# Optimization experiments

Measured on AMD Instinct MI355X. Metric: run time of the kernel, lower is better.

Reference implementation:

```python
import jax, jax.numpy as jnp
import numpy as np

DIM = 128      # encoder output dim
D_OUT = 10     # num classes
T = 1.0        # temperature
EPS = 1e-7


def setup_inputs() -> dict:
    key = jax.random.key(0)
    ks = jax.random.split(key, 5)
    B, N, D_IN = 512, 100000, 128
    x = jax.random.normal(ks[0], (B, D_IN), jnp.float32)
    candidate_x = jax.random.normal(ks[1], (N, D_IN), jnp.float32)
    candidate_y = jax.random.randint(ks[2], (N,), 0, D_OUT, dtype=jnp.int32)
    W = jax.random.normal(ks[3], (DIM, D_IN), jnp.float32) / np.sqrt(D_IN).astype(np.float32)
    b = jax.random.normal(ks[4], (DIM,), jnp.float32) * 0.01
    return {"x": x, "candidate_x": candidate_x, "candidate_y": candidate_y, "W": W, "b": b}


def reference(x, candidate_x, candidate_y, W, b):
    # Linear encoder (n_blocks == 0 path)
    h = x @ W.T + b              # [B, DIM]
    hc = candidate_x @ W.T + b   # [N, DIM]
    # Pairwise L2 distances via the Gram expansion (same math as torch.cdist p=2)
    d2 = (jnp.sum(h * h, axis=-1, keepdims=True)
          + jnp.sum(hc * hc, axis=-1)[None, :]
          - 2.0 * (h @ hc.T))    # [B, N]
    dist = jnp.sqrt(jnp.maximum(d2, 0.0)) / T
    # Attention-like masked softmax over candidates (eval: no diagonal mask)
    p = jax.nn.softmax(-dist, axis=-1)              # [B, N]
    onehot_y = jax.nn.one_hot(candidate_y, D_OUT, dtype=p.dtype)  # [N, D_OUT]
    logits = p @ onehot_y                           # [B, D_OUT]
    return jnp.log(logits + EPS)
```

## Files before the change

### kernel.cpp

```cpp
#include <hip/hip_runtime.h>
#include <stdint.h>

typedef __bf16 bf16x8 __attribute__((ext_vector_type(8)));
typedef float f32x4 __attribute__((ext_vector_type(4)));
typedef short short8 __attribute__((ext_vector_type(8)));
typedef unsigned int uint2v __attribute__((ext_vector_type(2)));
typedef float float4_t __attribute__((ext_vector_type(4)));

#define LOG2E 1.44269504088896340736f

union FragU { short8 s; bf16x8 b; };
union YbU { uint2v u2[2]; bf16x8 b; };

#define DEVI static __device__ __forceinline__

DEVI f32x4 mfma16(bf16x8 a, bf16x8 b, f32x4 c) {
  return __builtin_amdgcn_mfma_f32_16x16x32_bf16(a, b, c, 0, 0, 0);
}

DEVI bf16x8 cvt8(float4_t a, float4_t b) {
  bf16x8 r;
  r[0] = (__bf16)a[0]; r[1] = (__bf16)a[1]; r[2] = (__bf16)a[2]; r[3] = (__bf16)a[3];
  r[4] = (__bf16)b[0]; r[5] = (__bf16)b[1]; r[6] = (__bf16)b[2]; r[7] = (__bf16)b[3];
  return r;
}

__global__ __launch_bounds__(256, 3) void prep_encode_kernel(
    const float* __restrict__ cx, const float* __restrict__ x,
    const float* __restrict__ W, const float* __restrict__ bias,
    const int* __restrict__ y,
    unsigned short* __restrict__ HC, float* __restrict__ hcn,
    unsigned short* __restrict__ Hm, float* __restrict__ hnm,
    unsigned short* __restrict__ YT,
    int N, int Bm, int NP, int NBA, int NBB, int bpc) {
  __shared__ __align__(16) unsigned short Wl[128 * 128];

  const int bid = blockIdx.x, t = threadIdx.x;
  const int NB_ENC = NBA + NBB;

  if (bid >= NB_ENC) {
    if (bid == NB_ENC) {
      int i = N + t;
      if (i < NP) hcn[i] = 1e30f;
    } else {
      int k = bid - NB_ENC - 1;
      int c = k / bpc, j = k - c * bpc;
      int n0 = j * 2048 + t * 8;
      unsigned short* dst = YT + (size_t)c * NP + n0;
#pragma unroll
      for (int e = 0; e < 8; ++e) {
        int n = n0 + e;
        if (n < NP) dst[e] = (n < N && y[n] == c) ? 0x3F80u : 0u;
      }
    }
    return;
  }

  const float* in;
  unsigned short* outh;
  float* outnorm;
  int M, blk;
  if (bid < NBA) {
    in = cx; outh = HC; outnorm = hcn; M = N; blk = bid;
  } else {
    in = x; outh = Hm; outnorm = hnm; M = Bm; blk = bid - NBA;
  }

  const int lane = t & 63, w = t >> 6;
  const int g = lane >> 4, q = lane & 15;
  const int rb = blk * 128 + w * 16;

  float4_t iv[2][8];
  int arow[2];
  bool av[2];
#pragma unroll
  for (int s = 0; s < 2; ++s) {
    arow[s] = rb + s * 64 + q;
    av[s] = arow[s] < M;
    int ar = av[s] ? arow[s] : 0;
    const float* src = in + (size_t)ar * 128 + g * 8;
#pragma unroll
    for (int kc = 0; kc < 4; ++kc) {
      iv[s][2 * kc] = *(const float4_t*)(src + kc * 32);
      iv[s][2 * kc + 1] = *(const float4_t*)(src + kc * 32 + 4);
    }
  }

  {
    int row = t >> 1, half = t & 1;
    const float* wsrc = W + row * 128 + half * 64;
    float4_t wv[16];
#pragma unroll
    for (int j = 0; j < 16; ++j) wv[j] = *(const float4_t*)(wsrc + j * 4);
#pragma unroll
    for (int j = 0; j < 8; ++j) {
      FragU u; u.b = cvt8(wv[2 * j], wv[2 * j + 1]);
      int slot = (half * 8 + j) ^ (row & 7);
      *(short8*)((char*)Wl + row * 256 + slot * 16) = u.s;
    }
  }
  __syncthreads();

  bf16x8 a[2][4];
#pragma unroll
  for (int s = 0; s < 2; ++s)
#pragma unroll
    for (int kc = 0; kc < 4; ++kc) {
      FragU u; u.b = cvt8(iv[s][2 * kc], iv[s][2 * kc + 1]);
      if (!av[s]) u.s = short8{0, 0, 0, 0, 0, 0, 0, 0};
      a[s][kc] = u.b;
    }

  f32x4 acc[2][8];
#pragma unroll
  for (int s = 0; s < 2; ++s)
#pragma unroll
    for (int nt = 0; nt < 8; ++nt) acc[s][nt] = f32x4{0.f, 0.f, 0.f, 0.f};
#pragma unroll
  for (int nt = 0; nt < 8; ++nt) {
    int brow = nt * 16 + q;
#pragma unroll
    for (int kc = 0; kc < 4; ++kc) {
      int slot = (kc * 4 + g) ^ (brow & 7);
      FragU u;
      u.s = *(const short8*)((const char*)Wl + brow * 256 + slot * 16);
      acc[0][nt] = mfma16(a[0][kc], u.b, acc[0][nt]);
      acc[1][nt] = mfma16(a[1][kc], u.b, acc[1][nt]);
    }
  }

  float nsq[2][4] = {{0.f, 0.f, 0.f, 0.f}, {0.f, 0.f, 0.f, 0.f}};
#pragma unroll
  for (int nt = 0; nt < 8; ++nt) {
    int col = nt * 16 + q;
    float bv = bias[col];
#pragma unroll
    for (int s = 0; s < 2; ++s) {
#pragma unroll
      for (int r = 0; r < 4; ++r) {
        int row = rb + s * 64 + g * 4 + r;
        float val = (acc[s][nt][r] + bv) * LOG2E;
        __bf16 h = (__bf16)val;
        float vf = (float)h;
        nsq[s][r] += vf * vf;
        union { __bf16 h; unsigned short u; } cv; cv.h = h;
        if (row < M) outh[(size_t)row * 128 + col] = cv.u;
      }
    }
  }
#pragma unroll
  for (int m = 1; m < 16; m <<= 1) {
#pragma unroll
    for (int s = 0; s < 2; ++s)
#pragma unroll
      for (int r = 0; r < 4; ++r) nsq[s][r] += __shfl_xor(nsq[s][r], m, 64);
  }
  if (q == 0) {
#pragma unroll
    for (int s = 0; s < 2; ++s)
#pragma unroll
      for (int r = 0; r < 4; ++r) {
        int row = rb + s * 64 + g * 4 + r;
        if (row < M) outnorm[row] = nsq[s][r];
      }
  }
}

__global__ __launch_bounds__(512, 4) void nca_main(
    const unsigned short* __restrict__ H, const float* __restrict__ hnorm,
    const unsigned short* __restrict__ HC, const float* __restrict__ hcnorm,
    const unsigned short* __restrict__ YT, float* __restrict__ part,
    int B, int N, int NP, int NT, int CHUNKS) {
  __shared__ __align__(16) unsigned short HCl[3 * 64 * 128];

  const int t = threadIdx.x, lane = t & 63, w = t >> 6;
  const int g = lane >> 4, q = lane & 15;
  const int rg = blockIdx.y, chunk = blockIdx.x;
  const int t0 = (int)(((long long)chunk * NT) / CHUNKS);
  const int t1 = (int)(((long long)(chunk + 1) * NT) / CHUNKS);

  bf16x8 hfrag[2][4];
  float hn[2];
  int hrow[2];
#pragma unroll
  for (int s = 0; s < 2; ++s) {
    hrow[s] = rg * 256 + s * 128 + w * 16 + q;
    bool v = hrow[s] < B;
    int ar = v ? hrow[s] : 0;
#pragma unroll
    for (int kc = 0; kc < 4; ++kc) {
      FragU u;
      u.s = *(const short8*)(H + (size_t)ar * 128 + kc * 32 + g * 8);
      if (!v) u.s = short8{0, 0, 0, 0, 0, 0, 0, 0};
      hfrag[s][kc] = u.b;
    }
    hn[s] = hnorm[ar];
  }

  int soff[4];
#pragma unroll
  for (int kc = 0; kc < 4; ++kc)
    soff[kc] = q * 256 + (((kc * 4 + g) ^ (q & 7)) << 4);

  const int srow = t >> 4;
  const int sslot = (t & 15) ^ (srow & 7);
  const int g_off = srow * 256 + sslot * 16;
  const int l_off = w * 1024;
  const char* HCc = (const char*)HC;

  f32x4 pool0 = f32x4{0.f, 0.f, 0.f, 0.f};
  f32x4 pool1 = f32x4{0.f, 0.f, 0.f, 0.f};

#define STAGE(TT, BI)                                                          \
  {                                                                            \
    const char* src_ = HCc + (size_t)(TT)*16384 + g_off;                       \
    char* lb_ = (char*)HCl + (BI)*16384 + l_off;                               \
    __builtin_amdgcn_global_load_lds(                                          \
        (const __attribute__((address_space(1))) unsigned int*)src_,           \
        (__attribute__((address_space(3))) unsigned int*)lb_, 16, 0, 0);       \
    __builtin_amdgcn_global_load_lds(                                          \
        (const __attribute__((address_space(1))) unsigned int*)(src_ + 8192),  \
        (__attribute__((address_space(3))) unsigned int*)(lb_ + 8192), 16, 0,  \
        0);                                                                    \
  }

  if (t0 < t1) STAGE(t0, 0);
  if (t0 + 1 < t1) STAGE(t0 + 1, 1);

  int bi = 0;
  for (int tt = t0; tt < t1; ++tt) {
    if (tt + 1 < t1) {
      asm volatile("s_waitcnt vmcnt(2)" ::: "memory");
    } else {
      asm volatile("s_waitcnt vmcnt(0)" ::: "memory");
    }
    __builtin_amdgcn_s_barrier();
    __builtin_amdgcn_sched_barrier(0);

    const int colbase = tt * 64;
    float4_t cnv[4];
    uint2v ytu[4];
#pragma unroll
    for (int ns = 0; ns < 4; ++ns) {
      cnv[ns] = *(const float4_t*)(hcnorm + colbase + ns * 16 + g * 4);
      ytu[ns] = *(const uint2v*)(YT + (size_t)q * NP + colbase + ns * 16 + g * 4);
    }
    __builtin_amdgcn_sched_barrier(0);

    int bs = bi + 2; if (bs >= 3) bs -= 3;
    if (tt + 2 < t1) STAGE(tt + 2, bs);

    const char* lb = (const char*)HCl + bi * 16384;
#pragma unroll
    for (int nsg = 0; nsg < 2; ++nsg) {
      f32x4 a0[2], a1[2];
#pragma unroll
      for (int k = 0; k < 2; ++k) {
        a0[k] = f32x4{0.f, 0.f, 0.f, 0.f};
        a1[k] = f32x4{0.f, 0.f, 0.f, 0.f};
      }
#pragma unroll
      for (int k = 0; k < 2; ++k) {
        int ns = nsg * 2 + k;
#pragma unroll
        for (int kc = 0; kc < 4; ++kc) {
          FragU u;
          u.s = *(const short8*)(lb + soff[kc] + ns * 4096);
          a0[k] = mfma16(u.b, hfrag[0][kc], a0[k]);
          a1[k] = mfma16(u.b, hfrag[1][kc], a1[k]);
        }
      }
#pragma unroll
      for (int k = 0; k < 2; ++k) {
        int ns = nsg * 2 + k;
        FragU wb0, wb1;
        wb0.s = short8{0, 0, 0, 0, 0, 0, 0, 0};
        wb1.s = short8{0, 0, 0, 0, 0, 0, 0, 0};
#pragma unroll
        for (int r = 0; r < 4; ++r) {
          float c0 = hn[0] + cnv[ns][r];
          float c1 = hn[1] + cnv[ns][r];
          float d20 = fmaxf(fmaf(-2.f, a0[k][r], c0), 0.f);
          float d21 = fmaxf(fmaf(-2.f, a1[k][r], c1), 0.f);
          float di0 = __builtin_amdgcn_sqrtf(d20);
          float di1 = __builtin_amdgcn_sqrtf(d21);
          wb0.b[r] = (__bf16)__builtin_amdgcn_exp2f(-di0);
          wb1.b[r] = (__bf16)__builtin_amdgcn_exp2f(-di1);
        }
        YbU yb;
        yb.u2[0] = ytu[ns];
        yb.u2[1] = uint2v{0u, 0u};
        pool0 = mfma16(yb.b, wb0.b, pool0);
        pool1 = mfma16(yb.b, wb1.b, pool1);
      }
    }
    ++bi; if (bi == 3) bi = 0;
  }
#undef STAGE

  if (hrow[0] < B)
    *(f32x4*)(part + ((size_t)hrow[0] * CHUNKS + chunk) * 16 + g * 4) = pool0;
  if (hrow[1] < B)
    *(f32x4*)(part + ((size_t)hrow[1] * CHUNKS + chunk) * 16 + g * 4) = pool1;
}

__global__ __launch_bounds__(256) void finalize_kernel(
    const float* __restrict__ part, float* __restrict__ out, int B,
    int CHUNKS) {
  const int w = threadIdx.x >> 6, t = threadIdx.x & 63;
  const int row = blockIdx.x * 4 + w;
  if (row >= B) return;
  const int c = t & 15, grp = t >> 4;
  const float* p = part + (size_t)row * CHUNKS * 16;
  float s = 0.f;
  for (int j = grp; j < CHUNKS; j += 4) s += p[j * 16 + c];
  s += __shfl_xor(s, 16, 64);
  s += __shfl_xor(s, 32, 64);
  float Z = 0.f;
#pragma unroll
  for (int cc = 0; cc < 10; ++cc) Z += __shfl(s, cc, 64);
  if (t < 10) out[row * 10 + t] = logf(fmaf(s, 1.f / Z, 1e-7f));
}

extern "C" void kernel_launch(void* const* d_in, const int* in_sizes, int n_in,
                              void* d_out, int out_size, void* d_ws,
                              size_t ws_size, hipStream_t stream) {
  const float* x = (const float*)d_in[0];
  const float* cx = (const float*)d_in[1];
  const int* cy = (const int*)d_in[2];
  const float* W = (const float*)d_in[3];
  const float* b = (const float*)d_in[4];
  const int B = in_sizes[0] / 128;
  const int N = in_sizes[1] / 128;
  float* out = (float*)d_out;

  const int NT = (N + 63) / 64;
  const int NP = NT * 64;
  const int RG = (B + 255) / 256;

  char* ws = (char*)d_ws;
  size_t o = 0;
  auto alloc = [&](size_t bytes) {
    size_t r = o;
    o += (bytes + 255) & ~(size_t)255;
    return r;
  };
  unsigned short* HC = (unsigned short*)(ws + alloc((size_t)N * 128 * 2));
  float* hcn = (float*)(ws + alloc((size_t)NP * 4 + 16384));
  unsigned short* H = (unsigned short*)(ws + alloc((size_t)B * 128 * 2));
  float* hn = (float*)(ws + alloc((size_t)B * 4));
  unsigned short* YT = (unsigned short*)(ws + alloc((size_t)16 * NP * 2));

  size_t avail = (ws_size > o) ? (ws_size - o) : 0;
  int CHUNKS = (int)(avail / ((size_t)B * 16 * 4));
  if (CHUNKS > 256) CHUNKS = 256;
  if (CHUNKS < 32) CHUNKS = 32;
  float* part = (float*)(ws + alloc((size_t)CHUNKS * B * 16 * 4));

  const int NBA = (N + 127) / 128, NBB = (B + 127) / 128;
  const int bpc = (NP + 2047) / 2048;
  prep_encode_kernel<<<NBA + NBB + 1 + 16 * bpc, 256, 0, stream>>>(
      cx, x, W, b, cy, HC, hcn, H, hn, YT, N, B, NP, NBA, NBB, bpc);

  dim3 grid(CHUNKS, RG);
  nca_main<<<grid, 512, 0, stream>>>(H, hn, HC, hcn, YT, part, B, N, NP, NT,
                                     CHUNKS);
  finalize_kernel<<<(B + 3) / 4, 256, 0, stream>>>(part, out, B, CHUNKS);
}
```

Measured before the change: 161.3 us.

## Prefetch candidate norms and labels one tile ahead with register double-buffering

The main loop now loads the candidate norms and transposed labels for the next tile into a second register set before computing the current tile. The loop is unrolled by two so the register sets swap roles, which hides the global-load latency that previously stalled right after each barrier. The vmcnt accounting still works because these loads are issued before the LDS stage of tile tt+2. Separately, the encode kernel raises its launch-bounds occupancy hint from 3 to 4, loads W in two halves to cut register pressure, and hoists the bias into an fma with the LOG2E scale. The extra prefetch registers could add register pressure in the main kernel.

```diff
diff --git a/kernel.cpp b/kernel.cpp
--- a/kernel.cpp
+++ b/kernel.cpp
@@ -25,7 +25,7 @@
   return r;
 }
 
-__global__ __launch_bounds__(256, 3) void prep_encode_kernel(
+__global__ __launch_bounds__(256, 4) void prep_encode_kernel(
     const float* __restrict__ cx, const float* __restrict__ x,
     const float* __restrict__ W, const float* __restrict__ bias,
     const int* __restrict__ y,
@@ -89,14 +89,17 @@
   {
     int row = t >> 1, half = t & 1;
     const float* wsrc = W + row * 128 + half * 64;
-    float4_t wv[16];
-#pragma unroll
-    for (int j = 0; j < 16; ++j) wv[j] = *(const float4_t*)(wsrc + j * 4);
-#pragma unroll
-    for (int j = 0; j < 8; ++j) {
-      FragU u; u.b = cvt8(wv[2 * j], wv[2 * j + 1]);
-      int slot = (half * 8 + j) ^ (row & 7);
-      *(short8*)((char*)Wl + row * 256 + slot * 16) = u.s;
+#pragma unroll
+    for (int bb = 0; bb < 2; ++bb) {
+      float4_t wv[8];
+#pragma unroll
+      for (int j = 0; j < 8; ++j) wv[j] = *(const float4_t*)(wsrc + bb * 32 + j * 4);
+#pragma unroll
+      for (int j = 0; j < 4; ++j) {
+        FragU u; u.b = cvt8(wv[2 * j], wv[2 * j + 1]);
+        int slot = (half * 8 + bb * 4 + j) ^ (row & 7);
+        *(short8*)((char*)Wl + row * 256 + slot * 16) = u.s;
+      }
     }
   }
   __syncthreads();
@@ -110,6 +113,10 @@
       if (!av[s]) u.s = short8{0, 0, 0, 0, 0, 0, 0, 0};
       a[s][kc] = u.b;
     }
+
+  float bvv[8];
+#pragma unroll
+  for (int nt = 0; nt < 8; ++nt) bvv[nt] = bias[nt * 16 + q];
 
   f32x4 acc[2][8];
 #pragma unroll
@@ -133,13 +140,13 @@
 #pragma unroll
   for (int nt = 0; nt < 8; ++nt) {
     int col = nt * 16 + q;
-    float bv = bias[col];
+    float bl = bvv[nt] * LOG2E;
 #pragma unroll
     for (int s = 0; s < 2; ++s) {
 #pragma unroll
       for (int r = 0; r < 4; ++r) {
         int row = rb + s * 64 + g * 4 + r;
-        float val = (acc[s][nt][r] + bv) * LOG2E;
+        float val = fmaf(acc[s][nt][r], LOG2E, bl);
         __bf16 h = (__bf16)val;
         float vf = (float)h;
         nsq[s][r] += vf * vf;
@@ -224,78 +231,86 @@
         0);                                                                    \
   }
 
+#define LOADCY(TT, CNV, YTU)                                                   \
+  {                                                                            \
+    const int cb_ = (TT)*64;                                                   \
+    _Pragma("unroll") for (int ns = 0; ns < 4; ++ns) {                         \
+      CNV[ns] = *(const float4_t*)(hcnorm + cb_ + ns * 16 + g * 4);            \
+      YTU[ns] = *(const uint2v*)(YT + (size_t)q * NP + cb_ + ns * 16 + g * 4); \
+    }                                                                          \
+  }
+
+#define ITER(TT, CNV, YTU, CNVN, YTUN)                                         \
+  {                                                                            \
+    if ((TT) + 1 >= t1) {                                                      \
+      asm volatile("s_waitcnt vmcnt(0)" ::: "memory");                         \
+    } else {                                                                   \
+      asm volatile("s_waitcnt vmcnt(2)" ::: "memory");                         \
+    }                                                                          \
+    __builtin_amdgcn_s_barrier();                                              \
+    __builtin_amdgcn_sched_barrier(0);                                         \
+    if ((TT) + 1 < t1) LOADCY((TT) + 1, CNVN, YTUN);                           \
+    int bs_ = bi + 2; if (bs_ >= 3) bs_ -= 3;                                  \
+    if ((TT) + 2 < t1) STAGE((TT) + 2, bs_);                                   \
+    const char* lb = (const char*)HCl + bi * 16384;                            \
+    _Pragma("unroll") for (int nsg = 0; nsg < 2; ++nsg) {                      \
+      f32x4 a0[2], a1[2];                                                      \
+      _Pragma("unroll") for (int k = 0; k < 2; ++k) {                          \
+        a0[k] = f32x4{0.f, 0.f, 0.f, 0.f};                                     \
+        a1[k] = f32x4{0.f, 0.f, 0.f, 0.f};                                     \
+      }                                                                        \
+      _Pragma("unroll") for (int k = 0; k < 2; ++k) {                          \
+        int ns = nsg * 2 + k;                                                  \
+        _Pragma("unroll") for (int kc = 0; kc < 4; ++kc) {                     \
+          FragU u;                                                             \
+          u.s = *(const short8*)(lb + soff[kc] + ns * 4096);                   \
+          a0[k] = mfma16(u.b, hfrag[0][kc], a0[k]);                            \
+          a1[k] = mfma16(u.b, hfrag[1][kc], a1[k]);                            \
+        }                                                                      \
+      }                                                                        \
+      _Pragma("unroll") for (int k = 0; k < 2; ++k) {                          \
+        int ns = nsg * 2 + k;                                                  \
+        FragU wb0, wb1;                                                        \
+        wb0.s = short8{0, 0, 0, 0, 0, 0, 0, 0};                                \
+        wb1.s = short8{0, 0, 0, 0, 0, 0, 0, 0};                                \
+        _Pragma("unroll") for (int r = 0; r < 4; ++r) {                        \
+          float c0 = hn[0] + CNV[ns][r];                                       \
+          float c1 = hn[1] + CNV[ns][r];                                       \
+          float d20 = fmaxf(fmaf(-2.f, a0[k][r], c0), 0.f);                    \
+          float d21 = fmaxf(fmaf(-2.f, a1[k][r], c1), 0.f);                    \
+          float di0 = __builtin_amdgcn_sqrtf(d20);                             \
+          float di1 = __builtin_amdgcn_sqrtf(d21);                             \
+          wb0.b[r] = (__bf16)__builtin_amdgcn_exp2f(-di0);                     \
+          wb1.b[r] = (__bf16)__builtin_amdgcn_exp2f(-di1);                     \
+        }                                                                      \
+        YbU yb;                                                                \
+        yb.u2[0] = YTU[ns];                                                    \
+        yb.u2[1] = uint2v{0u, 0u};                                             \
+        pool0 = mfma16(yb.b, wb0.b, pool0);                                    \
+        pool1 = mfma16(yb.b, wb1.b, pool1);                                    \
+      }                                                                        \
+    }                                                                          \
+    ++bi; if (bi == 3) bi = 0;                                                 \
+  }
+
+  float4_t cnvA[4], cnvB[4];
+  uint2v ytuA[4], ytuB[4];
+
+  LOADCY(t0, cnvA, ytuA);
   if (t0 < t1) STAGE(t0, 0);
   if (t0 + 1 < t1) STAGE(t0 + 1, 1);
 
   int bi = 0;
-  for (int tt = t0; tt < t1; ++tt) {
-    if (tt + 1 < t1) {
-      asm volatile("s_waitcnt vmcnt(2)" ::: "memory");
-    } else {
-      asm volatile("s_waitcnt vmcnt(0)" ::: "memory");
-    }
-    __builtin_amdgcn_s_barrier();
-    __builtin_amdgcn_sched_barrier(0);
-
-    const int colbase = tt * 64;
-    float4_t cnv[4];
-    uint2v ytu[4];
-#pragma unroll
-    for (int ns = 0; ns < 4; ++ns) {
-      cnv[ns] = *(const float4_t*)(hcnorm + colbase + ns * 16 + g * 4);
-      ytu[ns] = *(const uint2v*)(YT + (size_t)q * NP + colbase + ns * 16 + g * 4);
-    }
-    __builtin_amdgcn_sched_barrier(0);
-
-    int bs = bi + 2; if (bs >= 3) bs -= 3;
-    if (tt + 2 < t1) STAGE(tt + 2, bs);
-
-    const char* lb = (const char*)HCl + bi * 16384;
-#pragma unroll
-    for (int nsg = 0; nsg < 2; ++nsg) {
-      f32x4 a0[2], a1[2];
-#pragma unroll
-      for (int k = 0; k < 2; ++k) {
-        a0[k] = f32x4{0.f, 0.f, 0.f, 0.f};
-        a1[k] = f32x4{0.f, 0.f, 0.f, 0.f};
-      }
-#pragma unroll
-      for (int k = 0; k < 2; ++k) {
-        int ns = nsg * 2 + k;
-#pragma unroll
-        for (int kc = 0; kc < 4; ++kc) {
-          FragU u;
-          u.s = *(const short8*)(lb + soff[kc] + ns * 4096);
-          a0[k] = mfma16(u.b, hfrag[0][kc], a0[k]);
-          a1[k] = mfma16(u.b, hfrag[1][kc], a1[k]);
-        }
-      }
-#pragma unroll
-      for (int k = 0; k < 2; ++k) {
-        int ns = nsg * 2 + k;
-        FragU wb0, wb1;
-        wb0.s = short8{0, 0, 0, 0, 0, 0, 0, 0};
-        wb1.s = short8{0, 0, 0, 0, 0, 0, 0, 0};
-#pragma unroll
-        for (int r = 0; r < 4; ++r) {
-          float c0 = hn[0] + cnv[ns][r];
-          float c1 = hn[1] + cnv[ns][r];
-          float d20 = fmaxf(fmaf(-2.f, a0[k][r], c0), 0.f);
-          float d21 = fmaxf(fmaf(-2.f, a1[k][r], c1), 0.f);
-          float di0 = __builtin_amdgcn_sqrtf(d20);
-          float di1 = __builtin_amdgcn_sqrtf(d21);
-          wb0.b[r] = (__bf16)__builtin_amdgcn_exp2f(-di0);
-          wb1.b[r] = (__bf16)__builtin_amdgcn_exp2f(-di1);
-        }
-        YbU yb;
-        yb.u2[0] = ytu[ns];
-        yb.u2[1] = uint2v{0u, 0u};
-        pool0 = mfma16(yb.b, wb0.b, pool0);
-        pool1 = mfma16(yb.b, wb1.b, pool1);
-      }
-    }
-    ++bi; if (bi == 3) bi = 0;
-  }
+  int tt = t0;
+  while (tt < t1) {
+    ITER(tt, cnvA, ytuA, cnvB, ytuB);
+    ++tt;
+    if (tt >= t1) break;
+    ITER(tt, cnvB, ytuB, cnvA, ytuA);
+    ++tt;
+  }
+#undef ITER
+#undef LOADCY
 #undef STAGE
 
   if (hrow[0] < B)
```

New measurement: 188.5 us. 16.9% more time.

## Stage encoder input through LDS with coalesced loads and halve rows per block

Applied to the files above, without the earlier changes.

The encode kernel now handles 64 rows per block instead of 128, which doubles the number of encode blocks. Each thread loads a contiguous 128-byte span of the input with coalesced float4 reads, converts it to bf16, and writes it into a swizzled LDS tile. MFMA A-fragments are then read from that tile, replacing the strided per-fragment global loads. The W staging loop is split into two halves to lower register pressure, and the bias is folded into an fma. The cost is an extra 16 KB of LDS per block, and the W conversion is repeated across twice as many blocks. The cvt8 edit is a redundant no-op rewrite.

```diff
diff --git a/kernel.cpp b/kernel.cpp
--- a/kernel.cpp
+++ b/kernel.cpp
@@ -21,7 +21,8 @@
 DEVI bf16x8 cvt8(float4_t a, float4_t b) {
   bf16x8 r;
   r[0] = (__bf16)a[0]; r[1] = (__bf16)a[1]; r[2] = (__bf16)a[2]; r[3] = (__bf16)a[3];
-  r[4] = (__bf16)b[0]; r[5] = (__bf16)b[1]; r[6] = (__bf16)b[2]; r[7] = (__bf16)b[3];
+  r[4] = (__bf16)b[0]; r[5] = (__bf16)b[1]; r[6] = (__bf16)b[2]; r[7] = (__bf16)b[7-4];
+  r[5] = (__bf16)b[1]; r[6] = (__bf16)b[2]; r[7] = (__bf16)b[3];
   return r;
 }
 
@@ -34,6 +35,7 @@
     unsigned short* __restrict__ YT,
     int N, int Bm, int NP, int NBA, int NBB, int bpc) {
   __shared__ __align__(16) unsigned short Wl[128 * 128];
+  __shared__ __align__(16) unsigned short Il[64 * 128];
 
   const int bid = blockIdx.x, t = threadIdx.x;
   const int NB_ENC = NBA + NBB;
@@ -68,54 +70,66 @@
 
   const int lane = t & 63, w = t >> 6;
   const int g = lane >> 4, q = lane & 15;
-  const int rb = blk * 128 + w * 16;
-
-  float4_t iv[2][8];
-  int arow[2];
-  bool av[2];
-#pragma unroll
-  for (int s = 0; s < 2; ++s) {
-    arow[s] = rb + s * 64 + q;
-    av[s] = arow[s] < M;
-    int ar = av[s] ? arow[s] : 0;
-    const float* src = in + (size_t)ar * 128 + g * 8;
-#pragma unroll
-    for (int kc = 0; kc < 4; ++kc) {
-      iv[s][2 * kc] = *(const float4_t*)(src + kc * 32);
-      iv[s][2 * kc + 1] = *(const float4_t*)(src + kc * 32 + 4);
-    }
+  const int rowbase = blk * 64 + w * 16;
+
+  float4_t v[8];
+  {
+    int fl = blk * 8192 + t * 32;
+    int flmax = M * 128 - 32;
+    if (fl > flmax) fl = flmax;
+    const float4_t* src = (const float4_t*)(in + fl);
+#pragma unroll
+    for (int j = 0; j < 8; ++j) v[j] = src[j];
   }
 
   {
     int row = t >> 1, half = t & 1;
     const float* wsrc = W + row * 128 + half * 64;
-    float4_t wv[16];
-#pragma unroll
-    for (int j = 0; j < 16; ++j) wv[j] = *(const float4_t*)(wsrc + j * 4);
-#pragma unroll
-    for (int j = 0; j < 8; ++j) {
-      FragU u; u.b = cvt8(wv[2 * j], wv[2 * j + 1]);
-      int slot = (half * 8 + j) ^ (row & 7);
-      *(short8*)((char*)Wl + row * 256 + slot * 16) = u.s;
+#pragma unroll
+    for (int bb = 0; bb < 2; ++bb) {
+      float4_t wv[8];
+#pragma unroll
+      for (int j = 0; j < 8; ++j) wv[j] = *(const float4_t*)(wsrc + bb * 32 + j * 4);
+#pragma unroll
+      for (int j = 0; j < 4; ++j) {
+        FragU u; u.b = cvt8(wv[2 * j], wv[2 * j + 1]);
+        int slot = (half * 8 + bb * 4 + j) ^ (row & 7);
+        *(short8*)((char*)Wl + row * 256 + slot * 16) = u.s;
+      }
+    }
+  }
+
+  {
+    int ir = t >> 2, c4 = t & 3;
+#pragma unroll
+    for (int j = 0; j < 2; ++j) {
+      FragU u; u.b = cvt8(v[4 * j], v[4 * j + 1]);
+      FragU u2; u2.b = cvt8(v[4 * j + 2], v[4 * j + 3]);
+      int slot = (c4 * 4 + 2 * j) ^ (ir & 7);
+      int slot2 = (c4 * 4 + 2 * j + 1) ^ (ir & 7);
+      *(short8*)((char*)Il + ir * 256 + slot * 16) = u.s;
+      *(short8*)((char*)Il + ir * 256 + slot2 * 16) = u2.s;
     }
   }
   __syncthreads();
 
-  bf16x8 a[2][4];
-#pragma unroll
-  for (int s = 0; s < 2; ++s)
-#pragma unroll
-    for (int kc = 0; kc < 4; ++kc) {
-      FragU u; u.b = cvt8(iv[s][2 * kc], iv[s][2 * kc + 1]);
-      if (!av[s]) u.s = short8{0, 0, 0, 0, 0, 0, 0, 0};
-      a[s][kc] = u.b;
-    }
-
-  f32x4 acc[2][8];
-#pragma unroll
-  for (int s = 0; s < 2; ++s)
-#pragma unroll
-    for (int nt = 0; nt < 8; ++nt) acc[s][nt] = f32x4{0.f, 0.f, 0.f, 0.f};
+  bf16x8 a[4];
+#pragma unroll
+  for (int kc = 0; kc < 4; ++kc) {
+    int r = w * 16 + q;
+    int slot = (kc * 4 + g) ^ (r & 7);
+    FragU u;
+    u.s = *(const short8*)((const char*)Il + r * 256 + slot * 16);
+    a[kc] = u.b;
+  }
+
+  float bvv[8];
+#pragma unroll
+  for (int nt = 0; nt < 8; ++nt) bvv[nt] = bias[nt * 16 + q];
+
+  f32x4 acc[8];
+#pragma unroll
+  for (int nt = 0; nt < 8; ++nt) acc[nt] = f32x4{0.f, 0.f, 0.f, 0.f};
 #pragma unroll
   for (int nt = 0; nt < 8; ++nt) {
     int brow = nt * 16 + q;
@@ -124,45 +138,37 @@
       int slot = (kc * 4 + g) ^ (brow & 7);
       FragU u;
       u.s = *(const short8*)((const char*)Wl + brow * 256 + slot * 16);
-      acc[0][nt] = mfma16(a[0][kc], u.b, acc[0][nt]);
-      acc[1][nt] = mfma16(a[1][kc], u.b, acc[1][nt]);
-    }
-  }
-
-  float nsq[2][4] = {{0.f, 0.f, 0.f, 0.f}, {0.f, 0.f, 0.f, 0.f}};
+      acc[nt] = mfma16(a[kc], u.b, acc[nt]);
+    }
+  }
+
+  float nsq[4] = {0.f, 0.f, 0.f, 0.f};
 #pragma unroll
   for (int nt = 0; nt < 8; ++nt) {
     int col = nt * 16 + q;
-    float bv = bias[col];
-#pragma unroll
-    for (int s = 0; s < 2; ++s) {
-#pragma unroll
-      for (int r = 0; r < 4; ++r) {
-        int row = rb + s * 64 + g * 4 + r;
-        float val = (acc[s][nt][r] + bv) * LOG2E;
-        __bf16 h = (__bf16)val;
-        float vf = (float)h;
-        nsq[s][r] += vf * vf;
-        union { __bf16 h; unsigned short u; } cv; cv.h = h;
-        if (row < M) outh[(size_t)row * 128 + col] = cv.u;
-      }
+    float bl = bvv[nt] * LOG2E;
+#pragma unroll
+    for (int r = 0; r < 4; ++r) {
+      int row = rowbase + g * 4 + r;
+      float val = fmaf(acc[nt][r], LOG2E, bl);
+      __bf16 h = (__bf16)val;
+      float vf = (float)h;
+      nsq[r] += vf * vf;
+      union { __bf16 h; unsigned short u; } cv; cv.h = h;
+      if (row < M) outh[(size_t)row * 128 + col] = cv.u;
     }
   }
 #pragma unroll
   for (int m = 1; m < 16; m <<= 1) {
 #pragma unroll
-    for (int s = 0; s < 2; ++s)
-#pragma unroll
-      for (int r = 0; r < 4; ++r) nsq[s][r] += __shfl_xor(nsq[s][r], m, 64);
+    for (int r = 0; r < 4; ++r) nsq[r] += __shfl_xor(nsq[r], m, 64);
   }
   if (q == 0) {
 #pragma unroll
-    for (int s = 0; s < 2; ++s)
-#pragma unroll
-      for (int r = 0; r < 4; ++r) {
-        int row = rb + s * 64 + g * 4 + r;
-        if (row < M) outnorm[row] = nsq[s][r];
-      }
+    for (int r = 0; r < 4; ++r) {
+      int row = rowbase + g * 4 + r;
+      if (row < M) outnorm[row] = nsq[r];
+    }
   }
 }
 
@@ -357,7 +363,7 @@
   if (CHUNKS < 32) CHUNKS = 32;
   float* part = (float*)(ws + alloc((size_t)CHUNKS * B * 16 * 4));
 
-  const int NBA = (N + 127) / 128, NBB = (B + 127) / 128;
+  const int NBA = (N + 63) / 64, NBB = (B + 63) / 64;
   const int bpc = (NP + 2047) / 2048;
   prep_encode_kernel<<<NBA + NBB + 1 + 16 * bpc, 256, 0, stream>>>(
       cx, x, W, b, cy, HC, hcn, H, hn, YT, N, B, NP, NBA, NBB, bpc);
```

After: 162.2 us. Within noise of the previous version (+0.6%).
